# Performance work log

Hardware: AMD Instinct MI355X
Metric: run time of the kernel (lower is better)

The kernel has to match this reference:

```python
import jax, jax.numpy as jnp
import numpy as np

D_MODEL = 1024
H = 16
D_K = D_MODEL // H

def setup_inputs() -> dict:
    key = jax.random.key(0)
    k1, k2, k3, k4, k5 = jax.random.split(key, 5)
    x = jax.random.normal(k1, (2, 2048, D_MODEL), dtype=jnp.float32)
    s = 1.0 / np.sqrt(D_MODEL)
    W_qkv = jax.random.uniform(k2, (D_MODEL, 3 * D_MODEL), jnp.float32, -s, s)
    b_qkv = jax.random.uniform(k3, (3 * D_MODEL,), jnp.float32, -s, s)
    W_o = jax.random.uniform(k4, (D_MODEL, D_MODEL), jnp.float32, -s, s)
    b_o = jax.random.uniform(k5, (D_MODEL,), jnp.float32, -s, s)
    return {"x": x, "W_qkv": W_qkv, "b_qkv": b_qkv, "W_o": W_o, "b_o": b_o}

def reference(x, W_qkv, b_qkv, W_o, b_o):
    B, L, _ = x.shape
    qkv = x @ W_qkv + b_qkv                      # [B, L, 3*d_model]
    q, k, v = jnp.split(qkv, 3, axis=-1)
    def split_heads(t):
        return t.reshape(B, L, H, D_K).transpose(0, 2, 1, 3)  # [B,H,L,D_k]
    q, k, v = split_heads(q), split_heads(k), split_heads(v)
    scores = jnp.einsum('bhqd,bhkd->bhqk', q, k) / np.sqrt(D_K).astype(jnp.float32)
    attn = jax.nn.softmax(scores, axis=-1)       # [B,H,L,L]
    ctx = jnp.einsum('bhqk,bhkd->bhqd', attn, v)
    ctx = ctx.transpose(0, 2, 1, 3).reshape(B, L, H * D_K)
    out = ctx @ W_o + b_o                        # dropout is identity at eval
    return (out, attn)
```

## Files before the change

### kernel.cpp

```cpp
#include <hip/hip_runtime.h>
#include <stdint.h>

typedef __attribute__((ext_vector_type(8))) short bf16x8;
typedef __attribute__((ext_vector_type(4))) float f32x4;
typedef __attribute__((ext_vector_type(4))) unsigned int u32x4;
typedef __attribute__((ext_vector_type(4))) unsigned short u16x4;

#define DEVINL static __device__ __forceinline__

DEVINL unsigned short f2bf(float f) {
  uint32_t u = __builtin_bit_cast(uint32_t, f);
  u = (u + 0x7FFFu + ((u >> 16) & 1u)) >> 16;
  return (unsigned short)u;
}

DEVINL float fexp2(float x) {
#if __has_builtin(__builtin_amdgcn_exp2f)
  return __builtin_amdgcn_exp2f(x);
#else
  return __expf(x * 0.69314718056f);
#endif
}

DEVINL void raw_barrier() {
  __builtin_amdgcn_sched_barrier(0);
  __builtin_amdgcn_s_barrier();
  __builtin_amdgcn_sched_barrier(0);
}

DEVINL void barrier_lds_only() {
  asm volatile("s_waitcnt lgkmcnt(0)" ::: "memory");
  raw_barrier();
}

DEVINL bf16x8 pack8(f32x4 a, f32x4 b) {
  union { uint32_t u[4]; bf16x8 v; } r;
  asm("v_cvt_pk_bf16_f32 %0, %1, %2" : "=v"(r.u[0]) : "v"(a[0]), "v"(a[1]));
  asm("v_cvt_pk_bf16_f32 %0, %1, %2" : "=v"(r.u[1]) : "v"(a[2]), "v"(a[3]));
  asm("v_cvt_pk_bf16_f32 %0, %1, %2" : "=v"(r.u[2]) : "v"(b[0]), "v"(b[1]));
  asm("v_cvt_pk_bf16_f32 %0, %1, %2" : "=v"(r.u[3]) : "v"(b[2]), "v"(b[3]));
  return r.v;
}

DEVINL void async16(const unsigned short* lds, const unsigned short* g) {
  __builtin_amdgcn_global_load_lds(
      (const __attribute__((address_space(1))) unsigned int*)g,
      (__attribute__((address_space(3))) unsigned int*)lds, 16, 0, 0);
}

__global__ __launch_bounds__(256) void k_cast_x(const float* __restrict__ in,
                                                unsigned short* __restrict__ out, int n4) {
  int i = blockIdx.x * 256 + threadIdx.x;
  if (i >= n4) return;
  f32x4 v = *(const f32x4*)(in + (size_t)i * 4);
  u16x4 o;
  for (int j = 0; j < 4; ++j) o[j] = f2bf(v[j]);
  *(u16x4*)(out + (size_t)i * 4) = o;
}

__global__ __launch_bounds__(256) void k_transpose_w(const float* __restrict__ in,
                                                     unsigned short* __restrict__ out,
                                                     int K, int N) {
  __shared__ unsigned short tile[64][72];
  int k0 = blockIdx.x * 64, n0 = blockIdx.y * 64;
  int t = threadIdx.x;
  int r = t >> 2, c0 = (t & 3) * 16;
  for (int j = 0; j < 4; ++j) {
    int col = c0 + j * 4;
    f32x4 v = *(const f32x4*)(in + (size_t)(k0 + r) * N + n0 + col);
    u16x4 o;
    for (int q = 0; q < 4; ++q) o[q] = f2bf(v[q]);
    *(u16x4*)(&tile[r][col]) = o;
  }
  __syncthreads();
  for (int j = 0; j < 4; ++j) {
    int kcol = c0 + j * 4;
    u16x4 o;
    for (int q = 0; q < 4; ++q) o[q] = tile[kcol + q][r];
    *(u16x4*)(out + (size_t)(n0 + r) * K + k0 + kcol) = o;
  }
}

template <int MODE>
__global__ __launch_bounds__(256) void k_gemm(const unsigned short* __restrict__ A,
                                              const unsigned short* __restrict__ Bt,
                                              const float* __restrict__ bias,
                                              unsigned short* __restrict__ Qb,
                                              unsigned short* __restrict__ Kb,
                                              unsigned short* __restrict__ Vt,
                                              float* __restrict__ outF) {
  constexpr int KD = 1024;
  __shared__ unsigned short sh[17408];
  unsigned short* lA = sh;
  unsigned short* lB = sh + 8192;
  int tid = threadIdx.x;
  int lane = tid & 63, w = tid >> 6;
  int wr = w >> 1, wc = w & 1;
  int m0 = blockIdx.x * 128, n0 = blockIdx.y * 128;
  int lr = lane & 15, lg = lane >> 4;

  f32x4 acc[4][4] = {};

  int srow = w * 32 + (lane >> 3);
  int scol = (lane & 7) * 8;
  const unsigned short* gA = A + (size_t)(m0 + srow) * KD + scol;
  const unsigned short* gB = Bt + (size_t)(n0 + srow) * KD + scol;

  for (int kk = 0; kk < KD; kk += 64) {
    for (int s = 0; s < 4; ++s) {
      async16(&lA[(w * 32 + s * 8) * 64], gA + (size_t)s * 8 * KD + kk);
      async16(&lB[(w * 32 + s * 8) * 64], gB + (size_t)s * 8 * KD + kk);
    }
    __syncthreads();
    for (int kq = 0; kq < 2; ++kq) {
      bf16x8 af[4], bfr[4];
      for (int i = 0; i < 4; ++i)
        af[i] = *(const bf16x8*)(&lA[(wr * 64 + i * 16 + lr) * 64 + (kq * 4 + lg) * 8]);
      for (int r = 0; r < 4; ++r)
        bfr[r] = *(const bf16x8*)(&lB[(wc * 64 + r * 16 + lr) * 64 + (kq * 4 + lg) * 8]);
      for (int i = 0; i < 4; ++i)
        for (int r = 0; r < 4; ++r)
          acc[i][r] = __builtin_amdgcn_mfma_f32_16x16x32_bf16(af[i], bfr[r], acc[i][r], 0, 0, 0);
    }
    __syncthreads();
  }

  if (MODE == 0) {
    int which = n0 >> 10;
    int head0 = (n0 & 1023) >> 6;
    int b_idx = m0 >> 11;
    int l0 = m0 & 2047;
    if (which < 2) {
      for (int r = 0; r < 4; ++r) {
        int nl = wc * 64 + r * 16 + lr;
        float bv = bias[n0 + nl];
        for (int i = 0; i < 4; ++i) {
          int mlb = wr * 64 + i * 16 + lg * 4;
          for (int jj = 0; jj < 4; ++jj)
            sh[(mlb + jj) * 136 + nl] = f2bf(acc[i][r][jj] + bv);
        }
      }
      __syncthreads();
      unsigned short* dst = (which == 0) ? Qb : Kb;
      for (int it = 0; it < 4; ++it) {
        int row = it * 64 + (tid >> 2);
        int ml = row & 127, hd = row >> 7;
        int c = (tid & 3) * 16;
        bf16x8 v0 = *(const bf16x8*)&sh[ml * 136 + hd * 64 + c];
        bf16x8 v1 = *(const bf16x8*)&sh[ml * 136 + hd * 64 + c + 8];
        size_t bh = (size_t)(b_idx * 16 + head0 + hd);
        size_t off = (bh * 2048 + l0 + ml) * 64 + c;
        *(bf16x8*)(dst + off) = v0;
        *(bf16x8*)(dst + off + 8) = v1;
      }
    } else {
      for (int r = 0; r < 4; ++r) {
        int nl = wc * 64 + r * 16 + lr;
        float bv = bias[n0 + nl];
        for (int i = 0; i < 4; ++i) {
          int mlb = wr * 64 + i * 16 + lg * 4;
          u16x4 pk;
          for (int jj = 0; jj < 4; ++jj) pk[jj] = f2bf(acc[i][r][jj] + bv);
          *(u16x4*)&sh[nl * 136 + mlb] = pk;
        }
      }
      __syncthreads();
      for (int it = 0; it < 4; ++it) {
        int nl = it * 32 + (tid >> 3);
        int c = (tid & 7) * 16;
        bf16x8 v0 = *(const bf16x8*)&sh[nl * 136 + c];
        bf16x8 v1 = *(const bf16x8*)&sh[nl * 136 + c + 8];
        int dk = nl & 63, hd = nl >> 6;
        size_t bh = (size_t)(b_idx * 16 + head0 + hd);
        size_t off = (bh * 64 + dk) * 2048 + l0 + c;
        *(bf16x8*)(Vt + off) = v0;
        *(bf16x8*)(Vt + off + 8) = v1;
      }
    }
  } else {
    for (int r = 0; r < 4; ++r) {
      int n = n0 + wc * 64 + r * 16 + lr;
      float bv = bias[n];
      for (int i = 0; i < 4; ++i) {
        int mb = m0 + wr * 64 + i * 16 + lg * 4;
        for (int jj = 0; jj < 4; ++jj)
          outF[(size_t)(mb + jj) * 1024 + n] = acc[i][r][jj] + bv;
      }
    }
  }
}

__global__ __launch_bounds__(256) void k_attn(const unsigned short* __restrict__ Qb,
                                              const unsigned short* __restrict__ Kb,
                                              const unsigned short* __restrict__ Vt,
                                              float* __restrict__ attn,
                                              unsigned short* __restrict__ ctx) {
  __shared__ unsigned short Ks[2][4096];
  __shared__ unsigned short Vs[2][4096];
  __shared__ float Pf[4][32 * 68];
  int tid = threadIdx.x, lane = tid & 63, w = tid >> 6;
  int lr = lane & 15, lg = lane >> 4;
  int bid = blockIdx.x;
  int xcd = bid & 7, slot = bid >> 3;
  int bh = xcd * 4 + (slot >> 4);
  int qb = slot & 15;
  int q0 = qb * 128 + w * 32;
  int b_idx = bh >> 4, h = bh & 15;
  const unsigned short* Qh = Qb + (size_t)bh * 2048 * 64;
  const unsigned short* Kh = Kb + (size_t)bh * 2048 * 64;
  const unsigned short* Vh = Vt + (size_t)bh * 64 * 2048;
  float* Pw = &Pf[w][0];
  const float A2 = 0.125f * 1.44269504089f;
  int e7 = lr & 7;

  int srow = w * 8 + (lane >> 3);
  int sc = (lane & 7) ^ (srow & 7);
  const unsigned short* gK = Kh + (size_t)srow * 64 + sc * 8;
  const unsigned short* gV = Vh + (size_t)srow * 2048 + sc * 8;

  bf16x8 qf[2][2];
  for (int i = 0; i < 2; ++i)
    for (int kq = 0; kq < 2; ++kq)
      qf[i][kq] = *(const bf16x8*)(Qh + (size_t)(q0 + i * 16 + lr) * 64 + kq * 32 + lg * 8);

  float l_run[8] = {0.f, 0.f, 0.f, 0.f, 0.f, 0.f, 0.f, 0.f};

  async16(&Ks[0][(w * 8) * 64],       gK);
  async16(&Ks[0][((w + 4) * 8) * 64], gK + 2048);
  for (int kt = 0; kt < 32; ++kt) {
    int cur = kt & 1;
    if (kt < 31) {
      async16(&Ks[cur ^ 1][(w * 8) * 64],       gK + (size_t)(kt + 1) * 4096);
      async16(&Ks[cur ^ 1][((w + 4) * 8) * 64], gK + (size_t)(kt + 1) * 4096 + 2048);
      asm volatile("s_waitcnt vmcnt(2)" ::: "memory");
    } else {
      asm volatile("s_waitcnt vmcnt(0)" ::: "memory");
    }
    raw_barrier();
    f32x4 acc[2][4] = {};
    for (int kq = 0; kq < 2; ++kq) {
      int j = kq * 4 + lg;
      bf16x8 kf[4];
      for (int r = 0; r < 4; ++r)
        kf[r] = *(const bf16x8*)&Ks[cur][(r * 16 + lr) * 64 + ((j ^ e7) << 3)];
      for (int i = 0; i < 2; ++i)
        for (int r = 0; r < 4; ++r)
          acc[i][r] = __builtin_amdgcn_mfma_f32_16x16x32_bf16(qf[i][kq], kf[r], acc[i][r], 0, 0, 0);
    }
    for (int i = 0; i < 2; ++i)
      for (int jj = 0; jj < 4; ++jj) {
        int z = i * 4 + jj;
        l_run[z] += fexp2(acc[i][0][jj] * A2) + fexp2(acc[i][1][jj] * A2) +
                    fexp2(acc[i][2][jj] * A2) + fexp2(acc[i][3][jj] * A2);
      }
    barrier_lds_only();
  }
  float invl[8];
  for (int z = 0; z < 8; ++z) {
    float s = l_run[z];
    s += __shfl_xor(s, 1);
    s += __shfl_xor(s, 2);
    s += __shfl_xor(s, 4);
    s += __shfl_xor(s, 8);
    invl[z] = 1.0f / s;
  }

  f32x4 cacc[2][4] = {};
  float* attn_base = attn + (size_t)bh * 2048 * 2048;
  float* arow = attn_base + (size_t)(q0 + lg) * 2048 + lr * 4;

  async16(&Ks[0][(w * 8) * 64],       gK);
  async16(&Ks[0][((w + 4) * 8) * 64], gK + 2048);
  async16(&Vs[0][(w * 8) * 64],       gV);
  async16(&Vs[0][((w + 4) * 8) * 64], gV + 65536);
  for (int kt = 0; kt < 32; ++kt) {
    int cur = kt & 1;
    if (kt < 31) {
      async16(&Ks[cur ^ 1][(w * 8) * 64],       gK + (size_t)(kt + 1) * 4096);
      async16(&Ks[cur ^ 1][((w + 4) * 8) * 64], gK + (size_t)(kt + 1) * 4096 + 2048);
      async16(&Vs[cur ^ 1][(w * 8) * 64],       gV + (size_t)(kt + 1) * 64);
      async16(&Vs[cur ^ 1][((w + 4) * 8) * 64], gV + (size_t)(kt + 1) * 64 + 65536);
    }
    if (kt == 0)       asm volatile("s_waitcnt vmcnt(4)" ::: "memory");
    else if (kt == 31) asm volatile("s_waitcnt vmcnt(8)" ::: "memory");
    else               asm volatile("s_waitcnt vmcnt(12)" ::: "memory");
    raw_barrier();
    f32x4 acc[2][4] = {};
    for (int kq = 0; kq < 2; ++kq) {
      int j = kq * 4 + lg;
      bf16x8 kf[4];
      for (int r = 0; r < 4; ++r)
        kf[r] = *(const bf16x8*)&Ks[cur][(r * 16 + lr) * 64 + ((j ^ e7) << 3)];
      for (int i = 0; i < 2; ++i)
        for (int r = 0; r < 4; ++r)
          acc[i][r] = __builtin_amdgcn_mfma_f32_16x16x32_bf16(qf[i][kq], kf[r], acc[i][r], 0, 0, 0);
    }
    for (int i = 0; i < 2; ++i)
      for (int r = 0; r < 4; ++r) {
        int key = r * 16 + lr;
        for (int jj = 0; jj < 4; ++jj) {
          int z = i * 4 + jj;
          int rl = i * 16 + lg * 4 + jj;
          Pw[rl * 68 + key] = fexp2(acc[i][r][jj] * A2) * invl[z];
        }
      }
    for (int s = 0; s < 8; ++s) {
      f32x4 v = *(const f32x4*)(&Pw[(s * 4 + lg) * 68 + lr * 4]);
      __builtin_nontemporal_store(v, (f32x4*)(arow + (size_t)s * 4 * 2048 + kt * 64));
    }
    for (int kq2 = 0; kq2 < 2; ++kq2) {
      int j = kq2 * 4 + lg;
      int kof = kq2 * 32 + lg * 8;
      bf16x8 pa[2], vf[4];
      for (int i = 0; i < 2; ++i) {
        f32x4 plo = *(const f32x4*)(&Pw[(i * 16 + lr) * 68 + kof]);
        f32x4 phi = *(const f32x4*)(&Pw[(i * 16 + lr) * 68 + kof + 4]);
        pa[i] = pack8(plo, phi);
      }
      for (int nn = 0; nn < 4; ++nn)
        vf[nn] = *(const bf16x8*)&Vs[cur][(nn * 16 + lr) * 64 + ((j ^ e7) << 3)];
      for (int i = 0; i < 2; ++i)
        for (int nn = 0; nn < 4; ++nn)
          cacc[i][nn] = __builtin_amdgcn_mfma_f32_16x16x32_bf16(pa[i], vf[nn], cacc[i][nn], 0, 0, 0);
    }
    barrier_lds_only();
  }

  for (int nn = 0; nn < 4; ++nn) {
    int d = nn * 16 + lr;
    for (int i = 0; i < 2; ++i)
      for (int jj = 0; jj < 4; ++jj) {
        int q = q0 + i * 16 + lg * 4 + jj;
        int tok = b_idx * 2048 + q;
        ctx[(size_t)tok * 1024 + h * 64 + d] = f2bf(cacc[i][nn][jj]);
      }
  }
}

extern "C" void kernel_launch(void* const* d_in, const int* in_sizes, int n_in,
                              void* d_out, int out_size, void* d_ws, size_t ws_size,
                              hipStream_t stream) {
  const float* x    = (const float*)d_in[0];
  const float* Wqkv = (const float*)d_in[1];
  const float* bqkv = (const float*)d_in[2];
  const float* Wo   = (const float*)d_in[3];
  const float* bo   = (const float*)d_in[4];
  float* out  = (float*)d_out;
  float* attn = out + (size_t)4096 * 1024;

  char* ws = (char*)d_ws;
  unsigned short* xbf = (unsigned short*)(ws);
  unsigned short* wqT = (unsigned short*)(ws + 8388608);
  unsigned short* woT = (unsigned short*)(ws + 14680064);
  unsigned short* Qb  = (unsigned short*)(ws + 16777216);
  unsigned short* Kb  = (unsigned short*)(ws + 25165824);
  unsigned short* Vt  = (unsigned short*)(ws + 33554432);
  unsigned short* ctx = (unsigned short*)(ws + 41943040);

  k_cast_x<<<dim3(4096), dim3(256), 0, stream>>>(x, xbf, 1048576);
  k_transpose_w<<<dim3(16, 48), dim3(256), 0, stream>>>(Wqkv, wqT, 1024, 3072);
  k_transpose_w<<<dim3(16, 16), dim3(256), 0, stream>>>(Wo, woT, 1024, 1024);
  k_gemm<0><<<dim3(32, 24), dim3(256), 0, stream>>>(xbf, wqT, bqkv, Qb, Kb, Vt, nullptr);
  k_attn<<<dim3(512), dim3(256), 0, stream>>>(Qb, Kb, Vt, attn, ctx);
  k_gemm<1><<<dim3(32, 8), dim3(256), 0, stream>>>(ctx, woT, bo, nullptr, nullptr, nullptr, out);
}
```

Baseline: 240.3 us.

## Merge prep kernels and swap MFMA operands to transpose score layout

```diff
diff --git a/kernel.cpp b/kernel.cpp
--- a/kernel.cpp
+++ b/kernel.cpp
@@ -48,22 +48,35 @@
       (__attribute__((address_space(3))) unsigned int*)lds, 16, 0, 0);
 }
 
-__global__ __launch_bounds__(256) void k_cast_x(const float* __restrict__ in,
-                                                unsigned short* __restrict__ out, int n4) {
-  int i = blockIdx.x * 256 + threadIdx.x;
-  if (i >= n4) return;
-  f32x4 v = *(const f32x4*)(in + (size_t)i * 4);
-  u16x4 o;
-  for (int j = 0; j < 4; ++j) o[j] = f2bf(v[j]);
-  *(u16x4*)(out + (size_t)i * 4) = o;
-}
-
-__global__ __launch_bounds__(256) void k_transpose_w(const float* __restrict__ in,
-                                                     unsigned short* __restrict__ out,
-                                                     int K, int N) {
+__global__ __launch_bounds__(256) void k_prep(const float* __restrict__ x,
+                                              unsigned short* __restrict__ xbf,
+                                              const float* __restrict__ Wqkv,
+                                              unsigned short* __restrict__ wqT,
+                                              const float* __restrict__ Wo,
+                                              unsigned short* __restrict__ woT) {
+  int bid = blockIdx.x;
+  int t = threadIdx.x;
+  if (bid < 4096) {
+    int i = bid * 256 + t;
+    f32x4 v = *(const f32x4*)(x + (size_t)i * 4);
+    u16x4 o;
+    for (int j = 0; j < 4; ++j) o[j] = f2bf(v[j]);
+    *(u16x4*)(xbf + (size_t)i * 4) = o;
+    return;
+  }
   __shared__ unsigned short tile[64][72];
-  int k0 = blockIdx.x * 64, n0 = blockIdx.y * 64;
-  int t = threadIdx.x;
+  const float* in;
+  unsigned short* out;
+  int K = 1024, N, k0, n0;
+  if (bid < 4864) {
+    int b = bid - 4096;
+    N = 3072; k0 = (b & 15) * 64; n0 = (b >> 4) * 64;
+    in = Wqkv; out = wqT;
+  } else {
+    int b = bid - 4864;
+    N = 1024; k0 = (b & 15) * 64; n0 = (b >> 4) * 64;
+    in = Wo; out = woT;
+  }
   int r = t >> 2, c0 = (t & 3) * 16;
   for (int j = 0; j < 4; ++j) {
     int col = c0 + j * 4;
@@ -223,7 +236,7 @@
     for (int kq = 0; kq < 2; ++kq)
       qf[i][kq] = *(const bf16x8*)(Qh + (size_t)(q0 + i * 16 + lr) * 64 + kq * 32 + lg * 8);
 
-  float l_run[8] = {0.f, 0.f, 0.f, 0.f, 0.f, 0.f, 0.f, 0.f};
+  float l_run[2] = {0.f, 0.f};
 
   async16(&Ks[0][(w * 8) * 64],       gK);
   async16(&Ks[0][((w + 4) * 8) * 64], gK + 2048);
@@ -245,24 +258,20 @@
         kf[r] = *(const bf16x8*)&Ks[cur][(r * 16 + lr) * 64 + ((j ^ e7) << 3)];
       for (int i = 0; i < 2; ++i)
         for (int r = 0; r < 4; ++r)
-          acc[i][r] = __builtin_amdgcn_mfma_f32_16x16x32_bf16(qf[i][kq], kf[r], acc[i][r], 0, 0, 0);
+          acc[i][r] = __builtin_amdgcn_mfma_f32_16x16x32_bf16(kf[r], qf[i][kq], acc[i][r], 0, 0, 0);
     }
     for (int i = 0; i < 2; ++i)
-      for (int jj = 0; jj < 4; ++jj) {
-        int z = i * 4 + jj;
-        l_run[z] += fexp2(acc[i][0][jj] * A2) + fexp2(acc[i][1][jj] * A2) +
-                    fexp2(acc[i][2][jj] * A2) + fexp2(acc[i][3][jj] * A2);
-      }
+      for (int r = 0; r < 4; ++r)
+        l_run[i] += fexp2(acc[i][r][0] * A2) + fexp2(acc[i][r][1] * A2) +
+                    fexp2(acc[i][r][2] * A2) + fexp2(acc[i][r][3] * A2);
     barrier_lds_only();
   }
-  float invl[8];
-  for (int z = 0; z < 8; ++z) {
-    float s = l_run[z];
-    s += __shfl_xor(s, 1);
-    s += __shfl_xor(s, 2);
-    s += __shfl_xor(s, 4);
-    s += __shfl_xor(s, 8);
-    invl[z] = 1.0f / s;
+  float invl[2];
+  for (int i = 0; i < 2; ++i) {
+    float s = l_run[i];
+    s += __shfl_xor(s, 16);
+    s += __shfl_xor(s, 32);
+    invl[i] = 1.0f / s;
   }
 
   f32x4 cacc[2][4] = {};
@@ -293,16 +302,14 @@
         kf[r] = *(const bf16x8*)&Ks[cur][(r * 16 + lr) * 64 + ((j ^ e7) << 3)];
       for (int i = 0; i < 2; ++i)
         for (int r = 0; r < 4; ++r)
-          acc[i][r] = __builtin_amdgcn_mfma_f32_16x16x32_bf16(qf[i][kq], kf[r], acc[i][r], 0, 0, 0);
+          acc[i][r] = __builtin_amdgcn_mfma_f32_16x16x32_bf16(kf[r], qf[i][kq], acc[i][r], 0, 0, 0);
     }
     for (int i = 0; i < 2; ++i)
       for (int r = 0; r < 4; ++r) {
-        int key = r * 16 + lr;
-        for (int jj = 0; jj < 4; ++jj) {
-          int z = i * 4 + jj;
-          int rl = i * 16 + lg * 4 + jj;
-          Pw[rl * 68 + key] = fexp2(acc[i][r][jj] * A2) * invl[z];
-        }
+        f32x4 pv;
+        for (int jj = 0; jj < 4; ++jj)
+          pv[jj] = fexp2(acc[i][r][jj] * A2) * invl[i];
+        *(f32x4*)&Pw[(i * 16 + lr) * 68 + r * 16 + lg * 4] = pv;
       }
     for (int s = 0; s < 8; ++s) {
       f32x4 v = *(const f32x4*)(&Pw[(s * 4 + lg) * 68 + lr * 4]);
@@ -357,9 +364,7 @@
   unsigned short* Vt  = (unsigned short*)(ws + 33554432);
   unsigned short* ctx = (unsigned short*)(ws + 41943040);
 
-  k_cast_x<<<dim3(4096), dim3(256), 0, stream>>>(x, xbf, 1048576);
-  k_transpose_w<<<dim3(16, 48), dim3(256), 0, stream>>>(Wqkv, wqT, 1024, 3072);
-  k_transpose_w<<<dim3(16, 16), dim3(256), 0, stream>>>(Wo, woT, 1024, 1024);
+  k_prep<<<dim3(5120), dim3(256), 0, stream>>>(x, xbf, Wqkv, wqT, Wo, woT);
   k_gemm<0><<<dim3(32, 24), dim3(256), 0, stream>>>(xbf, wqT, bqkv, Qb, Kb, Vt, nullptr);
   k_attn<<<dim3(512), dim3(256), 0, stream>>>(Qb, Kb, Vt, attn, ctx);
   k_gemm<1><<<dim3(32, 8), dim3(256), 0, stream>>>(ctx, woT, bo, nullptr, nullptr, nullptr, out);
```

After: 232.9 us. 3.1% less time.
